# Kernel optimization log

Hardware: AMD Instinct MI355X
Metric: run time of the kernel (lower is better)

Reference implementation:

```python
import jax, jax.numpy as jnp
import numpy as np

B, T, C = 4, 2048, 2048
N_HEAD = 16
HEAD_DIM = C // N_HEAD  # 128


def _apply_rotary_emb(x, cos, sin):
    # x: (B, T, H, D), cos/sin: (1, T, 1, D/2)
    d = x.shape[-1] // 2
    x1, x2 = x[..., :d], x[..., d:]
    return jnp.concatenate([x1 * cos + x2 * sin, -x2 * sin + x1 * cos], axis=-1)


def setup_inputs() -> dict:
    key = jax.random.key(0)
    ks = jax.random.split(key, 7)
    s = 0.02
    return {
        "x": jax.random.normal(ks[0], (B, T, C), dtype=jnp.float32),
        "cos": jax.random.normal(ks[1], (1, T, 1, HEAD_DIM // 2), dtype=jnp.float32),
        "sin": jax.random.normal(ks[2], (1, T, 1, HEAD_DIM // 2), dtype=jnp.float32),
        "wq": jax.random.normal(ks[3], (C, C), dtype=jnp.float32) * s,
        "wk": jax.random.normal(ks[4], (C, C), dtype=jnp.float32) * s,
        "wv": jax.random.normal(ks[5], (C, C), dtype=jnp.float32) * s,
        "wo": jax.random.normal(ks[6], (C, C), dtype=jnp.float32) * s,
    }


def reference(x, cos, sin, wq, wk, wv, wo):
    b, t, c = x.shape
    h, d = N_HEAD, HEAD_DIM
    # linear projections (torch Linear: x @ W.T), reshape to (B, T, H, D)
    q = (x @ wq.T).reshape(b, t, h, d)
    k = (x @ wk.T).reshape(b, t, h, d)
    v = (x @ wv.T).reshape(b, t, h, d)
    q = _apply_rotary_emb(q, cos, sin)
    k = _apply_rotary_emb(k, cos, sin)
    # scaled dot-product attention, non-causal; heads on axis 2
    scale = 1.0 / jnp.sqrt(jnp.float32(d))
    scores = jnp.einsum("bqhd,bkhd->bhqk", q, k) * scale
    attn = jax.nn.softmax(scores, axis=-1)
    y = jnp.einsum("bhqk,bkhd->bqhd", attn, v).reshape(b, t, c)
    return y @ wo.T
```

## Files before the change

kernel.cpp:

```cpp
#include <hip/hip_runtime.h>

#define B_SZ 4
#define T_SZ 2048
#define C_SZ 2048
#define H_SZ 16
#define D_SZ 128

typedef __attribute__((ext_vector_type(8))) __bf16 bf16x8;
typedef __attribute__((ext_vector_type(4))) float f32x4;
typedef __attribute__((ext_vector_type(4))) unsigned short us4;

static __device__ __forceinline__ unsigned short f2bf(float f) {
  unsigned u = __builtin_bit_cast(unsigned, f);
  u += 0x7fffu + ((u >> 16) & 1u);
  return (unsigned short)(u >> 16);
}

static __device__ __forceinline__ void gload16(const void* g, void* l) {
  __builtin_amdgcn_global_load_lds((__attribute__((address_space(1))) void*)(g),
                                   (__attribute__((address_space(3))) void*)(l), 16, 0, 0);
}

__global__ __launch_bounds__(256) void cast_f32_bf16(const float* __restrict__ src,
                                                     unsigned short* __restrict__ dst, int n4) {
  int i = blockIdx.x * 256 + threadIdx.x;
  if (i >= n4) return;
  float4 v = ((const float4*)src)[i];
  us4 o;
  o[0] = f2bf(v.x); o[1] = f2bf(v.y); o[2] = f2bf(v.z); o[3] = f2bf(v.w);
  ((us4*)dst)[i] = o;
}

template <int EPI>
__global__ __launch_bounds__(256) void gemm_bt(const unsigned short* __restrict__ A,
                                               const unsigned short* __restrict__ W,
                                               void* __restrict__ out,
                                               const float* __restrict__ cosp,
                                               const float* __restrict__ sinp,
                                               float outScale, int M, int N, int K) {
  __shared__ unsigned short As[128 * 32];
  __shared__ unsigned short Bs[128 * 32];
  const int tid = threadIdx.x;
  const int wave = tid >> 6, lane = tid & 63, quad = lane >> 4, l15 = lane & 15;
  const int m0 = blockIdx.y * 128, n0 = blockIdx.x * 128;
  f32x4 acc[2][8] = {};
  for (int kt = 0; kt < K; kt += 32) {
    __syncthreads();
#pragma unroll
    for (int s = 0; s < 2; ++s) {
      int i = s * 256 + tid;
      int row = i >> 2, pos = i & 3, c = pos ^ (row & 3);
      gload16(A + (size_t)(m0 + row) * K + kt + c * 8, (char*)As + i * 16);
      gload16(W + (size_t)(n0 + row) * K + kt + c * 8, (char*)Bs + i * 16);
    }
    __syncthreads();
    const int sw = (quad ^ (l15 & 3)) * 8;
    bf16x8 a0 = *(const bf16x8*)&As[(wave * 32 + l15) * 32 + sw];
    bf16x8 a1 = *(const bf16x8*)&As[(wave * 32 + 16 + l15) * 32 + sw];
#pragma unroll
    for (int nt = 0; nt < 8; ++nt) {
      bf16x8 b = *(const bf16x8*)&Bs[(nt * 16 + l15) * 32 + sw];
      acc[0][nt] = __builtin_amdgcn_mfma_f32_16x16x32_bf16(a0, b, acc[0][nt], 0, 0, 0);
      acc[1][nt] = __builtin_amdgcn_mfma_f32_16x16x32_bf16(a1, b, acc[1][nt], 0, 0, 0);
    }
  }
  const int mb = m0 + wave * 32;
  if (EPI == 1) {
    unsigned short* O = (unsigned short*)out;
#pragma unroll
    for (int mt = 0; mt < 2; ++mt)
#pragma unroll
      for (int r = 0; r < 4; ++r) {
        int m = mb + mt * 16 + quad * 4 + r;
        int t = m & (T_SZ - 1);
#pragma unroll
        for (int nt = 0; nt < 4; ++nt) {
          int dd = nt * 16 + l15;
          float c = cosp[t * 64 + dd];
          float s = sinp[t * 64 + dd];
          float x1 = acc[mt][nt][r], x2 = acc[mt][nt + 4][r];
          O[(size_t)m * N + n0 + dd]      = f2bf((x1 * c + x2 * s) * outScale);
          O[(size_t)m * N + n0 + dd + 64] = f2bf((x1 * c - x2 * s) * outScale);
        }
      }
  } else if (EPI == 2) {
    unsigned short* O = (unsigned short*)out;
#pragma unroll
    for (int mt = 0; mt < 2; ++mt) {
      int m4 = mb + mt * 16 + quad * 4;
      int bb = m4 >> 11;
      int t = m4 & (T_SZ - 1);
#pragma unroll
      for (int nt = 0; nt < 8; ++nt) {
        int n = n0 + nt * 16 + l15;
        int h = n >> 7, d = n & (D_SZ - 1);
        us4 pk;
        pk[0] = f2bf(acc[mt][nt][0]);
        pk[1] = f2bf(acc[mt][nt][1]);
        pk[2] = f2bf(acc[mt][nt][2]);
        pk[3] = f2bf(acc[mt][nt][3]);
        *(us4*)&O[((size_t)((bb * H_SZ + h) * D_SZ + d)) * T_SZ + t] = pk;
      }
    }
  } else {
    float* O = (float*)out;
#pragma unroll
    for (int mt = 0; mt < 2; ++mt)
#pragma unroll
      for (int nt = 0; nt < 8; ++nt)
#pragma unroll
        for (int r = 0; r < 4; ++r) {
          int m = mb + mt * 16 + quad * 4 + r;
          O[(size_t)m * N + n0 + nt * 16 + l15] = acc[mt][nt][r];
        }
  }
}

static __device__ __forceinline__ void stage_kv(const unsigned short* __restrict__ Kg,
                                                const unsigned short* __restrict__ Vt,
                                                unsigned short* Kbuf, unsigned short* Vbuf,
                                                size_t kbase0, size_t vbase0, int kt, int tid) {
  size_t kb = kbase0 + (size_t)kt * 64 * C_SZ;
  size_t vb = vbase0 + (size_t)kt * 64;
#pragma unroll
  for (int s = 0; s < 4; ++s) {
    int ii = s * 256 + tid;
    int krow = ii >> 4, kpos = ii & 15, kc = kpos ^ (krow & 15);
    gload16(Kg + kb + (size_t)krow * C_SZ + kc * 8, (char*)Kbuf + ii * 16);
    int vrow = ii >> 3, vpos = ii & 7, vc = vpos ^ (vrow & 7);
    gload16(Vt + vb + (size_t)vrow * T_SZ + vc * 8, (char*)Vbuf + ii * 16);
  }
}

__global__ __launch_bounds__(256, 2) void attn_fused(const unsigned short* __restrict__ Q,
                                                     const unsigned short* __restrict__ Kg,
                                                     const unsigned short* __restrict__ Vt,
                                                     unsigned short* __restrict__ Y) {
  __shared__ unsigned short Ks[2][64 * 128];
  __shared__ unsigned short Vs[2][128 * 64];
  __shared__ unsigned short Ps[4][32 * 40];
  const int tid = threadIdx.x;
  const int wave = tid >> 6, lane = tid & 63, quad = lane >> 4, l15 = lane & 15;
  const int kh = wave & 1, qh = wave >> 1;
  const int qt = blockIdx.x, bh = blockIdx.y;
  const int b = bh >> 4, h = bh & 15;
  const float LOG2E = 1.44269504088896f;

  bf16x8 aq[2][4];
  {
    size_t qrow0 = (size_t)(b * T_SZ + qt * 64 + qh * 32);
#pragma unroll
    for (int nt = 0; nt < 2; ++nt)
#pragma unroll
      for (int ks = 0; ks < 4; ++ks)
        aq[nt][ks] = *(const bf16x8*)(Q + (qrow0 + nt * 16 + l15) * C_SZ + h * D_SZ + ks * 32 + quad * 8);
  }

  const size_t kbase0 = ((size_t)(b * T_SZ)) * C_SZ + h * D_SZ;
  const size_t vbase0 = ((size_t)(bh * D_SZ)) * T_SZ;
  stage_kv(Kg, Vt, Ks[0], Vs[0], kbase0, vbase0, 0, tid);
  stage_kv(Kg, Vt, Ks[1], Vs[1], kbase0, vbase0, 1, tid);

  float mstate[2] = {-1e30f, -1e30f}, lstate[2] = {0.f, 0.f};
  f32x4 o[8][2] = {};
  unsigned short* PsW = Ps[wave];
  __syncthreads();

  for (int jt = 0; jt < T_SZ / 128; ++jt) {
    bf16x8 bkA[2][4], bvA[8];
#pragma unroll
    for (int mt = 0; mt < 2; ++mt)
#pragma unroll
      for (int ks = 0; ks < 4; ++ks)
        bkA[mt][ks] = *(const bf16x8*)&Ks[0][(kh * 32 + mt * 16 + l15) * 128 + (((ks * 4 + quad) ^ l15) * 8)];
#pragma unroll
    for (int dt = 0; dt < 8; ++dt)
      bvA[dt] = *(const bf16x8*)&Vs[0][(dt * 16 + l15) * 64 + (((kh * 4 + quad) ^ (l15 & 7)) * 8)];
    f32x4 sfA[2][2] = {};
#pragma unroll
    for (int mt = 0; mt < 2; ++mt)
#pragma unroll
      for (int ks = 0; ks < 4; ++ks)
#pragma unroll
        for (int nt = 0; nt < 2; ++nt)
          sfA[mt][nt] = __builtin_amdgcn_mfma_f32_16x16x32_bf16(bkA[mt][ks], aq[nt][ks], sfA[mt][nt], 0, 0, 0);
    __syncthreads();
    if (jt + 1 < T_SZ / 128) stage_kv(Kg, Vt, Ks[0], Vs[0], kbase0, vbase0, 2 * jt + 2, tid);
    bf16x8 bkB[2][4], bvB[8];
#pragma unroll
    for (int mt = 0; mt < 2; ++mt)
#pragma unroll
      for (int ks = 0; ks < 4; ++ks)
        bkB[mt][ks] = *(const bf16x8*)&Ks[1][(kh * 32 + mt * 16 + l15) * 128 + (((ks * 4 + quad) ^ l15) * 8)];
#pragma unroll
    for (int dt = 0; dt < 8; ++dt)
      bvB[dt] = *(const bf16x8*)&Vs[1][(dt * 16 + l15) * 64 + (((kh * 4 + quad) ^ (l15 & 7)) * 8)];
    f32x4 sfB[2][2] = {};
#pragma unroll
    for (int mt = 0; mt < 2; ++mt)
#pragma unroll
      for (int ks = 0; ks < 4; ++ks)
#pragma unroll
        for (int nt = 0; nt < 2; ++nt)
          sfB[mt][nt] = __builtin_amdgcn_mfma_f32_16x16x32_bf16(bkB[mt][ks], aq[nt][ks], sfB[mt][nt], 0, 0, 0);
    float alpha[2], rsum[2];
#pragma unroll
    for (int nt = 0; nt < 2; ++nt) {
      float rmax = sfA[0][nt][0];
#pragma unroll
      for (int mt = 0; mt < 2; ++mt)
#pragma unroll
        for (int r = 0; r < 4; ++r) {
          rmax = fmaxf(rmax, sfA[mt][nt][r]);
          rmax = fmaxf(rmax, sfB[mt][nt][r]);
        }
      rmax = fmaxf(rmax, __shfl_xor(rmax, 16));
      rmax = fmaxf(rmax, __shfl_xor(rmax, 32));
      float mnew = fmaxf(mstate[nt], rmax);
      alpha[nt] = exp2f((mstate[nt] - mnew) * LOG2E);
      mstate[nt] = mnew;
      rsum[nt] = 0.f;
    }
#pragma unroll
    for (int dt = 0; dt < 8; ++dt)
#pragma unroll
      for (int nt = 0; nt < 2; ++nt)
        o[dt][nt] *= alpha[nt];
#pragma unroll
    for (int nt = 0; nt < 2; ++nt)
#pragma unroll
      for (int mt = 0; mt < 2; ++mt) {
        us4 pk;
        float p0 = exp2f((sfA[mt][nt][0] - mstate[nt]) * LOG2E);
        float p1 = exp2f((sfA[mt][nt][1] - mstate[nt]) * LOG2E);
        float p2 = exp2f((sfA[mt][nt][2] - mstate[nt]) * LOG2E);
        float p3 = exp2f((sfA[mt][nt][3] - mstate[nt]) * LOG2E);
        rsum[nt] += (p0 + p1) + (p2 + p3);
        pk[0] = f2bf(p0); pk[1] = f2bf(p1); pk[2] = f2bf(p2); pk[3] = f2bf(p3);
        *(us4*)&PsW[(nt * 16 + l15) * 40 + mt * 16 + quad * 4] = pk;
      }
    {
      bf16x8 ap[2];
#pragma unroll
      for (int nt = 0; nt < 2; ++nt)
        ap[nt] = *(const bf16x8*)&PsW[(nt * 16 + l15) * 40 + quad * 8];
#pragma unroll
      for (int dt = 0; dt < 8; ++dt)
#pragma unroll
        for (int nt = 0; nt < 2; ++nt)
          o[dt][nt] = __builtin_amdgcn_mfma_f32_16x16x32_bf16(bvA[dt], ap[nt], o[dt][nt], 0, 0, 0);
    }
    asm volatile("" ::: "memory");
#pragma unroll
    for (int nt = 0; nt < 2; ++nt)
#pragma unroll
      for (int mt = 0; mt < 2; ++mt) {
        us4 pk;
        float p0 = exp2f((sfB[mt][nt][0] - mstate[nt]) * LOG2E);
        float p1 = exp2f((sfB[mt][nt][1] - mstate[nt]) * LOG2E);
        float p2 = exp2f((sfB[mt][nt][2] - mstate[nt]) * LOG2E);
        float p3 = exp2f((sfB[mt][nt][3] - mstate[nt]) * LOG2E);
        rsum[nt] += (p0 + p1) + (p2 + p3);
        pk[0] = f2bf(p0); pk[1] = f2bf(p1); pk[2] = f2bf(p2); pk[3] = f2bf(p3);
        *(us4*)&PsW[(nt * 16 + l15) * 40 + mt * 16 + quad * 4] = pk;
      }
    {
      bf16x8 ap[2];
#pragma unroll
      for (int nt = 0; nt < 2; ++nt)
        ap[nt] = *(const bf16x8*)&PsW[(nt * 16 + l15) * 40 + quad * 8];
#pragma unroll
      for (int dt = 0; dt < 8; ++dt)
#pragma unroll
        for (int nt = 0; nt < 2; ++nt)
          o[dt][nt] = __builtin_amdgcn_mfma_f32_16x16x32_bf16(bvB[dt], ap[nt], o[dt][nt], 0, 0, 0);
    }
#pragma unroll
    for (int nt = 0; nt < 2; ++nt) {
      rsum[nt] += __shfl_xor(rsum[nt], 16);
      rsum[nt] += __shfl_xor(rsum[nt], 32);
      lstate[nt] = lstate[nt] * alpha[nt] + rsum[nt];
    }
    __syncthreads();
    if (jt + 1 < T_SZ / 128) stage_kv(Kg, Vt, Ks[1], Vs[1], kbase0, vbase0, 2 * jt + 3, tid);
  }

  float* Xch = (float*)Ks;
  float* st  = (float*)Vs;
  if (kh == 1) {
#pragma unroll
    for (int dt = 0; dt < 8; ++dt)
#pragma unroll
      for (int nt = 0; nt < 2; ++nt)
        *(f32x4*)&Xch[((qh * 16 + dt * 2 + nt) * 64 + lane) * 4] = o[dt][nt];
    if (quad == 0) {
#pragma unroll
      for (int nt = 0; nt < 2; ++nt) {
        int q = qh * 32 + nt * 16 + l15;
        st[q] = mstate[nt];
        st[64 + q] = lstate[nt];
      }
    }
  }
  __syncthreads();
  if (kh == 0) {
#pragma unroll
    for (int nt = 0; nt < 2; ++nt) {
      int q = qh * 32 + nt * 16 + l15;
      float m1 = st[q], l1 = st[64 + q];
      float M = fmaxf(mstate[nt], m1);
      float a0 = exp2f((mstate[nt] - M) * LOG2E);
      float a1 = exp2f((m1 - M) * LOG2E);
      float L = lstate[nt] * a0 + l1 * a1;
      float inv = 1.0f / L;
      size_t row = (size_t)(b * T_SZ + qt * 64) + q;
#pragma unroll
      for (int dt = 0; dt < 8; ++dt) {
        f32x4 o1 = *(const f32x4*)&Xch[((qh * 16 + dt * 2 + nt) * 64 + lane) * 4];
        us4 pk;
        pk[0] = f2bf((o[dt][nt][0] * a0 + o1[0] * a1) * inv);
        pk[1] = f2bf((o[dt][nt][1] * a0 + o1[1] * a1) * inv);
        pk[2] = f2bf((o[dt][nt][2] * a0 + o1[2] * a1) * inv);
        pk[3] = f2bf((o[dt][nt][3] * a0 + o1[3] * a1) * inv);
        *(us4*)&Y[row * C_SZ + h * D_SZ + dt * 16 + quad * 4] = pk;
      }
    }
  }
}

extern "C" void kernel_launch(void* const* d_in, const int* in_sizes, int n_in,
                              void* d_out, int out_size, void* d_ws, size_t ws_size,
                              hipStream_t stream) {
  (void)in_sizes; (void)n_in; (void)out_size; (void)ws_size;
  const float* x    = (const float*)d_in[0];
  const float* cosp = (const float*)d_in[1];
  const float* sinp = (const float*)d_in[2];
  const float* wq   = (const float*)d_in[3];
  const float* wk   = (const float*)d_in[4];
  const float* wv   = (const float*)d_in[5];
  const float* wo   = (const float*)d_in[6];
  float* out = (float*)d_out;

  const size_t XE = (size_t)B_SZ * T_SZ * C_SZ;
  const size_t WE = (size_t)C_SZ * C_SZ;
  unsigned short* Xb = (unsigned short*)d_ws;
  unsigned short* Qb = Xb + XE;
  unsigned short* Kb = Qb + XE;
  unsigned short* Vt = Kb + XE;
  unsigned short* Wb = Vt + XE;
  unsigned short* Y  = Xb;

  const int M = B_SZ * T_SZ, N = C_SZ, K = C_SZ;
  dim3 ggrid(N / 128, M / 128);
  int nbx = (int)(XE / 4 / 256);
  int nbw = (int)(WE / 4 / 256);
  const float qscale = 0.088388347648318447f;

  cast_f32_bf16<<<nbx, 256, 0, stream>>>(x, Xb, (int)(XE / 4));

  cast_f32_bf16<<<nbw, 256, 0, stream>>>(wq, Wb, (int)(WE / 4));
  gemm_bt<1><<<ggrid, 256, 0, stream>>>(Xb, Wb, Qb, cosp, sinp, qscale, M, N, K);

  cast_f32_bf16<<<nbw, 256, 0, stream>>>(wk, Wb, (int)(WE / 4));
  gemm_bt<1><<<ggrid, 256, 0, stream>>>(Xb, Wb, Kb, cosp, sinp, 1.0f, M, N, K);

  cast_f32_bf16<<<nbw, 256, 0, stream>>>(wv, Wb, (int)(WE / 4));
  gemm_bt<2><<<ggrid, 256, 0, stream>>>(Xb, Wb, Vt, nullptr, nullptr, 1.0f, M, N, K);

  attn_fused<<<dim3(T_SZ / 64, B_SZ * H_SZ), 256, 0, stream>>>(Qb, Kb, Vt, Y);

  cast_f32_bf16<<<nbw, 256, 0, stream>>>(wo, Wb, (int)(WE / 4));
  gemm_bt<3><<<ggrid, 256, 0, stream>>>(Y, Wb, out, nullptr, nullptr, 1.0f, M, N, K);
}
```

Before: 847.4 us.

## Rewrite projection GEMM with 256x256 tiles and triple-buffered async LDS loads

```diff
diff --git a/kernel.cpp b/kernel.cpp
--- a/kernel.cpp
+++ b/kernel.cpp
@@ -31,87 +31,121 @@
   ((us4*)dst)[i] = o;
 }
 
+#define VM_SYNC(N)                                            \
+  do {                                                        \
+    asm volatile("s_waitcnt vmcnt(" #N ")" ::: "memory");     \
+    __builtin_amdgcn_s_barrier();                             \
+    asm volatile("" ::: "memory");                            \
+    __builtin_amdgcn_sched_barrier(0);                        \
+  } while (0)
+
 template <int EPI>
-__global__ __launch_bounds__(256) void gemm_bt(const unsigned short* __restrict__ A,
-                                               const unsigned short* __restrict__ W,
-                                               void* __restrict__ out,
-                                               const float* __restrict__ cosp,
-                                               const float* __restrict__ sinp,
-                                               float outScale, int M, int N, int K) {
-  __shared__ unsigned short As[128 * 32];
-  __shared__ unsigned short Bs[128 * 32];
+__global__ __launch_bounds__(512, 2) void gemm_bt(const unsigned short* __restrict__ A,
+                                                  const unsigned short* __restrict__ W,
+                                                  void* __restrict__ out,
+                                                  const float* __restrict__ cosp,
+                                                  const float* __restrict__ sinp,
+                                                  float outScale, int M, int N, int K) {
+  __shared__ unsigned short As[3][8192];
+  __shared__ unsigned short Bs[3][8192];
   const int tid = threadIdx.x;
   const int wave = tid >> 6, lane = tid & 63, quad = lane >> 4, l15 = lane & 15;
-  const int m0 = blockIdx.y * 128, n0 = blockIdx.x * 128;
-  f32x4 acc[2][8] = {};
-  for (int kt = 0; kt < K; kt += 32) {
-    __syncthreads();
-#pragma unroll
-    for (int s = 0; s < 2; ++s) {
-      int i = s * 256 + tid;
-      int row = i >> 2, pos = i & 3, c = pos ^ (row & 3);
-      gload16(A + (size_t)(m0 + row) * K + kt + c * 8, (char*)As + i * 16);
-      gload16(W + (size_t)(n0 + row) * K + kt + c * 8, (char*)Bs + i * 16);
-    }
-    __syncthreads();
-    const int sw = (quad ^ (l15 & 3)) * 8;
-    bf16x8 a0 = *(const bf16x8*)&As[(wave * 32 + l15) * 32 + sw];
-    bf16x8 a1 = *(const bf16x8*)&As[(wave * 32 + 16 + l15) * 32 + sw];
-#pragma unroll
-    for (int nt = 0; nt < 8; ++nt) {
-      bf16x8 b = *(const bf16x8*)&Bs[(nt * 16 + l15) * 32 + sw];
-      acc[0][nt] = __builtin_amdgcn_mfma_f32_16x16x32_bf16(a0, b, acc[0][nt], 0, 0, 0);
-      acc[1][nt] = __builtin_amdgcn_mfma_f32_16x16x32_bf16(a1, b, acc[1][nt], 0, 0, 0);
-    }
-  }
-  const int mb = m0 + wave * 32;
+  const int wm = wave >> 1, wn = wave & 1;
+  const int m0 = blockIdx.y * 256, n0 = blockIdx.x * 256;
+  const int NT = K >> 5;
+
+  const int c0 = tid, c1 = tid + 512;
+  const unsigned short* a0p = A + (size_t)(m0 + (c0 & 255)) * K + (c0 >> 8) * 8;
+  const unsigned short* a1p = A + (size_t)(m0 + (c1 & 255)) * K + (c1 >> 8) * 8;
+  const unsigned short* b0p = W + (size_t)(n0 + (c0 & 255)) * K + (c0 >> 8) * 8;
+  const unsigned short* b1p = W + (size_t)(n0 + (c1 & 255)) * K + (c1 >> 8) * 8;
+
+  f32x4 acc[4][8] = {};
+
+#define STAGE(t)                                        \
+  do {                                                  \
+    int kk = (t) * 32, sl = (t) % 3;                    \
+    gload16(a0p + kk, (char*)As[sl] + c0 * 16);         \
+    gload16(a1p + kk, (char*)As[sl] + c1 * 16);         \
+    gload16(b0p + kk, (char*)Bs[sl] + c0 * 16);         \
+    gload16(b1p + kk, (char*)Bs[sl] + c1 * 16);         \
+  } while (0)
+
+  STAGE(0);
+  STAGE(1);
+  VM_SYNC(4);
+
+  for (int t = 0; t < NT; ++t) {
+    if (t + 2 < NT) STAGE(t + 2);
+    const int sl = t % 3;
+    const int qo = quad * 2048;
+    bf16x8 af[4], bfr[8];
+#pragma unroll
+    for (int mf = 0; mf < 4; ++mf)
+      af[mf] = *(const bf16x8*)&As[sl][qo + (wm * 64 + mf * 16 + l15) * 8];
+#pragma unroll
+    for (int nf = 0; nf < 8; ++nf)
+      bfr[nf] = *(const bf16x8*)&Bs[sl][qo + (wn * 128 + nf * 16 + l15) * 8];
+    __builtin_amdgcn_s_setprio(1);
+#pragma unroll
+    for (int nf = 0; nf < 8; ++nf)
+#pragma unroll
+      for (int mf = 0; mf < 4; ++mf)
+        acc[mf][nf] = __builtin_amdgcn_mfma_f32_16x16x32_bf16(af[mf], bfr[nf], acc[mf][nf], 0, 0, 0);
+    __builtin_amdgcn_s_setprio(0);
+    if (t + 2 < NT) VM_SYNC(4);
+    else if (t + 1 < NT) VM_SYNC(0);
+  }
+#undef STAGE
+
+  const int mb = m0 + wm * 64, nb = n0 + wn * 128;
   if (EPI == 1) {
     unsigned short* O = (unsigned short*)out;
 #pragma unroll
-    for (int mt = 0; mt < 2; ++mt)
+    for (int mf = 0; mf < 4; ++mf)
 #pragma unroll
       for (int r = 0; r < 4; ++r) {
-        int m = mb + mt * 16 + quad * 4 + r;
-        int t = m & (T_SZ - 1);
-#pragma unroll
-        for (int nt = 0; nt < 4; ++nt) {
-          int dd = nt * 16 + l15;
-          float c = cosp[t * 64 + dd];
-          float s = sinp[t * 64 + dd];
-          float x1 = acc[mt][nt][r], x2 = acc[mt][nt + 4][r];
-          O[(size_t)m * N + n0 + dd]      = f2bf((x1 * c + x2 * s) * outScale);
-          O[(size_t)m * N + n0 + dd + 64] = f2bf((x1 * c - x2 * s) * outScale);
+        int m = mb + mf * 16 + quad * 4 + r;
+        int tt = m & (T_SZ - 1);
+#pragma unroll
+        for (int nf = 0; nf < 4; ++nf) {
+          int dd = nf * 16 + l15;
+          float c = cosp[tt * 64 + dd];
+          float s = sinp[tt * 64 + dd];
+          float x1 = acc[mf][nf][r], x2 = acc[mf][nf + 4][r];
+          O[(size_t)m * N + nb + dd]      = f2bf((x1 * c + x2 * s) * outScale);
+          O[(size_t)m * N + nb + dd + 64] = f2bf((x1 * c - x2 * s) * outScale);
         }
       }
   } else if (EPI == 2) {
     unsigned short* O = (unsigned short*)out;
 #pragma unroll
-    for (int mt = 0; mt < 2; ++mt) {
-      int m4 = mb + mt * 16 + quad * 4;
+    for (int mf = 0; mf < 4; ++mf) {
+      int m4 = mb + mf * 16 + quad * 4;
       int bb = m4 >> 11;
-      int t = m4 & (T_SZ - 1);
-#pragma unroll
-      for (int nt = 0; nt < 8; ++nt) {
-        int n = n0 + nt * 16 + l15;
+      int tt = m4 & (T_SZ - 1);
+#pragma unroll
+      for (int nf = 0; nf < 8; ++nf) {
+        int n = nb + nf * 16 + l15;
         int h = n >> 7, d = n & (D_SZ - 1);
         us4 pk;
-        pk[0] = f2bf(acc[mt][nt][0]);
-        pk[1] = f2bf(acc[mt][nt][1]);
-        pk[2] = f2bf(acc[mt][nt][2]);
-        pk[3] = f2bf(acc[mt][nt][3]);
-        *(us4*)&O[((size_t)((bb * H_SZ + h) * D_SZ + d)) * T_SZ + t] = pk;
+        pk[0] = f2bf(acc[mf][nf][0]);
+        pk[1] = f2bf(acc[mf][nf][1]);
+        pk[2] = f2bf(acc[mf][nf][2]);
+        pk[3] = f2bf(acc[mf][nf][3]);
+        *(us4*)&O[((size_t)((bb * H_SZ + h) * D_SZ + d)) * T_SZ + tt] = pk;
       }
     }
   } else {
     float* O = (float*)out;
 #pragma unroll
-    for (int mt = 0; mt < 2; ++mt)
-#pragma unroll
-      for (int nt = 0; nt < 8; ++nt)
+    for (int mf = 0; mf < 4; ++mf)
+#pragma unroll
+      for (int nf = 0; nf < 8; ++nf)
 #pragma unroll
         for (int r = 0; r < 4; ++r) {
-          int m = mb + mt * 16 + quad * 4 + r;
-          O[(size_t)m * N + n0 + nt * 16 + l15] = acc[mt][nt][r];
+          int m = mb + mf * 16 + quad * 4 + r;
+          O[(size_t)m * N + nb + nf * 16 + l15] = acc[mf][nf][r];
         }
   }
 }
@@ -351,7 +385,7 @@
   unsigned short* Y  = Xb;
 
   const int M = B_SZ * T_SZ, N = C_SZ, K = C_SZ;
-  dim3 ggrid(N / 128, M / 128);
+  dim3 ggrid(N / 256, M / 256);
   int nbx = (int)(XE / 4 / 256);
   int nbw = (int)(WE / 4 / 256);
   const float qscale = 0.088388347648318447f;
@@ -359,16 +393,16 @@
   cast_f32_bf16<<<nbx, 256, 0, stream>>>(x, Xb, (int)(XE / 4));
 
   cast_f32_bf16<<<nbw, 256, 0, stream>>>(wq, Wb, (int)(WE / 4));
-  gemm_bt<1><<<ggrid, 256, 0, stream>>>(Xb, Wb, Qb, cosp, sinp, qscale, M, N, K);
+  gemm_bt<1><<<ggrid, 512, 0, stream>>>(Xb, Wb, Qb, cosp, sinp, qscale, M, N, K);
 
   cast_f32_bf16<<<nbw, 256, 0, stream>>>(wk, Wb, (int)(WE / 4));
-  gemm_bt<1><<<ggrid, 256, 0, stream>>>(Xb, Wb, Kb, cosp, sinp, 1.0f, M, N, K);
+  gemm_bt<1><<<ggrid, 512, 0, stream>>>(Xb, Wb, Kb, cosp, sinp, 1.0f, M, N, K);
 
   cast_f32_bf16<<<nbw, 256, 0, stream>>>(wv, Wb, (int)(WE / 4));
-  gemm_bt<2><<<ggrid, 256, 0, stream>>>(Xb, Wb, Vt, nullptr, nullptr, 1.0f, M, N, K);
+  gemm_bt<2><<<ggrid, 512, 0, stream>>>(Xb, Wb, Vt, nullptr, nullptr, 1.0f, M, N, K);
 
   attn_fused<<<dim3(T_SZ / 64, B_SZ * H_SZ), 256, 0, stream>>>(Qb, Kb, Vt, Y);
 
   cast_f32_bf16<<<nbw, 256, 0, stream>>>(wo, Wb, (int)(WE / 4));
-  gemm_bt<3><<<ggrid, 256, 0, stream>>>(Y, Wb, out, nullptr, nullptr, 1.0f, M, N, K);
-}
+  gemm_bt<3><<<ggrid, 512, 0, stream>>>(Y, Wb, out, nullptr, nullptr, 1.0f, M, N, K);
+}
```

New measurement: 939.1 us. +10.8%, slower.
